# Kernel optimization log

Measured on AMD Instinct MI355X. Metric: run time of the kernel, lower is better.

## Reference

```python
import jax, jax.numpy as jnp
import numpy as np

DECAY = 0.1
ALPHA = 0.2
EPS = 1e-8


def setup_inputs() -> dict:
    key = jax.random.key(0)
    k1, k2, k3, k4 = jax.random.split(key, 4)
    B, S, N, V = 8, 1024, 64, 32000
    input_ids = jax.random.randint(k1, (B, S), 0, V)
    emb = jax.random.normal(k2, (V, N), dtype=jnp.float32)
    W = jax.random.normal(k3, (N, N, N), dtype=jnp.float32) * 0.05
    Wd = jax.random.normal(k4, (V, N), dtype=jnp.float32) * 0.02
    bd = jnp.zeros((V,), dtype=jnp.float32)
    return {"input_ids": input_ids, "emb": emb, "W": W, "Wd": Wd, "bd": bd}


def reference(input_ids, emb, W, Wd, bd):
    B, S = input_ids.shape
    N = W.shape[0]
    # Precompute relu(embedding) for all timesteps: [B, S, N]
    word = jax.nn.relu(emb[input_ids])

    def step(hidden, w_t):
        # hidden, w_t: [B, N]
        x = (1.0 - DECAY) * hidden + w_t
        interaction = jnp.einsum('ijk,bi,bj->bk', W, x, x)
        x_act = jax.nn.relu(x + ALPHA * interaction)
        h = x_act / (jnp.sum(x_act, axis=1, keepdims=True) + EPS)
        return h, h

    h0 = jnp.zeros((B, N), dtype=emb.dtype)
    hT, hs = jax.lax.scan(step, h0, jnp.swapaxes(word, 0, 1))  # hs: [S, B, N]
    # Decode every step: Linear(N -> V): h @ Wd.T + bd -> [B, S, V]
    logits = jnp.einsum('sbn,vn->bsv', hs, Wd) + bd
    return logits, hT
```

## Files before the change

kernel.cpp:

```cpp
#include <hip/hip_runtime.h>


typedef unsigned int u32;
typedef unsigned short u16;
typedef __attribute__((ext_vector_type(8))) short short8;
typedef __attribute__((ext_vector_type(4))) float f32x4;
typedef __attribute__((ext_vector_type(4))) int i32x4;

#define DECAY_ 0.1f
#define ALPHA_ 0.2f
#define EPS_ 1e-8f
#define B_ 8
#define S_ 1024
#define N_ 64
#define V_ 32000
#define NCHUNK_ 32
#define CHUNK_ 32
#define WARM_ 12
#define WBOUND_ 0.32f

static __device__ __forceinline__ u16 f2bf(float f) {
  u32 u = __float_as_uint(f);
  u32 r = (u + 0x7fffu + ((u >> 16) & 1u)) >> 16;
  return (u16)r;
}

#if defined(__has_builtin)
#if __has_builtin(__builtin_amdgcn_sdot4)
#define HAVE_SDOT4 1
#endif
#endif
static __device__ __forceinline__ int dot4(int a, int b, int c) {
#ifdef HAVE_SDOT4
  return __builtin_amdgcn_sdot4(a, b, c, false);
#else
  int s = c;
  s += (int)(signed char)(a) * (int)(signed char)(b);
  s += (int)(signed char)(a >> 8) * (int)(signed char)(b >> 8);
  s += (int)(signed char)(a >> 16) * (int)(signed char)(b >> 16);
  s += (int)(a >> 24) * (int)(b >> 24);
  return s;
#endif
}

static __device__ __forceinline__ float wave_max64(float v) {
#pragma unroll
  for (int m = 1; m < 64; m <<= 1) v = fmaxf(v, __shfl_xor(v, m, 64));
  return v;
}

__global__ void prep_kernel(const float* __restrict__ Wd, u16* __restrict__ wdb,
                            const float* __restrict__ W, u32* __restrict__ Wq) {
  int idx = blockIdx.x * blockDim.x + threadIdx.x;
  wdb[idx] = f2bf(Wd[idx]);
  if (blockIdx.x < 256) {
    const float s = 127.0f / WBOUND_;
    int j = idx >> 10;
    int q = (idx >> 6) & 15;
    int k = idx & 63;
    u32 pk = 0;
#pragma unroll
    for (int e = 0; e < 4; ++e) {
      float v = W[(((4 * q + e) * N_) + j) * N_ + k];
      int qi = (int)rintf(v * s);
      qi = qi > 127 ? 127 : (qi < -127 ? -127 : qi);
      pk |= ((u32)qi & 0xffu) << (8 * e);
    }
    int g = j >> 2, r = j & 3;
    int jX = g * 2 + (r & 1);
    int base = (r < 2) ? 0 : 32768;
    int q4 = q >> 2, e2 = q & 3;
    Wq[base + (((jX * 4 + q4) * 64 + k) << 2) + e2] = pk;
  }
}

__global__ __launch_bounds__(512, 2) void recur_kernel(
    const int* __restrict__ ids, const float* __restrict__ emb,
    const u32* __restrict__ Wq,
    u16* __restrict__ hs, float* __restrict__ outHT) {
  const int b = blockIdx.y;
  const int chunk = blockIdx.x;
  const int lane = threadIdx.x & 63;
  const int w = threadIdx.x >> 6;

  const int t0 = chunk * CHUNK_;
  const int ts = (chunk == 0) ? 0 : t0 - WARM_;
  const int tend = t0 + CHUNK_;

  __shared__ i32x4 lw[8192];
  __shared__ float part[8 * 64];
  __shared__ float xf_lds[N_];
  __shared__ u32 xq_lds[16];
  __shared__ float pend_w[2][N_];
  __shared__ float pend_b[2];

  const float sW = WBOUND_ * (1.0f / 127.0f);
  const i32x4* __restrict__ WqA = (const i32x4*)Wq;

  {
    const i32x4* src = (const i32x4*)(Wq + 32768);
    for (int ii = threadIdx.x; ii < 8192; ii += 512) lw[ii] = src[ii];
  }

  float xk = 0.0f, smul = 0.0f;

  if (w == 0) {
    int id0 = ids[b * S_ + ts];
    xk = fmaxf(emb[(size_t)id0 * N_ + lane], 0.0f);
    float bnd = fmaxf(wave_max64(xk), 1e-20f);
    smul = bnd * (1.0f / 127.0f) * sW;
    float inv = 127.0f / bnd;
    float u = xk * inv;
    float u0 = __shfl(u, (lane & 15) * 4 + 0, 64);
    float u1 = __shfl(u, (lane & 15) * 4 + 1, 64);
    float u2 = __shfl(u, (lane & 15) * 4 + 2, 64);
    float u3 = __shfl(u, (lane & 15) * 4 + 3, 64);
    xf_lds[lane] = xk;
    if (lane < 16) {
      xq_lds[lane] = (u32)(int)rintf(u0) | ((u32)(int)rintf(u1) << 8) |
                     ((u32)(int)rintf(u2) << 16) | ((u32)(int)rintf(u3) << 24);
    }
  }
  if (w == 1) {
    int i1 = ts + 1 < S_ ? ts + 1 : S_ - 1;
    int id1 = ids[b * S_ + i1];
    float pv = fmaxf(emb[(size_t)id1 * N_ + lane], 0.0f);
    float pm = wave_max64(pv);
    pend_w[(ts + 1) & 1][lane] = pv;
    if (lane == 0) pend_b[(ts + 1) & 1] = pm;
  }
  __syncthreads();

  for (int t = ts; t < tend; ++t) {
    float pv = 0.0f;
    if (w == 1) {
      int i2 = t + 2 < S_ ? t + 2 : S_ - 1;
      pv = emb[(size_t)ids[b * S_ + i2] * N_ + lane];
    }
    u32 pkv = xq_lds[lane & 15];
    int xr[16];
#pragma unroll
    for (int q = 0; q < 16; ++q) xr[q] = __builtin_amdgcn_readlane((int)pkv, q);
    float pf = 0.0f;
#pragma unroll
    for (int rr = 0; rr < 4; ++rr) {
      int a = 0;
#pragma unroll
      for (int q4 = 0; q4 < 4; ++q4) {
        i32x4 v = lw[((4 * w + rr) * 4 + q4) * 64 + lane];
        a = dot4(xr[4 * q4 + 0], v[0], a);
        a = dot4(xr[4 * q4 + 1], v[1], a);
        a = dot4(xr[4 * q4 + 2], v[2], a);
        a = dot4(xr[4 * q4 + 3], v[3], a);
      }
      int jb = (rr & 1) + ((rr & 2) << 1) + 2;
      pf += (float)a * xf_lds[8 * w + jb];
    }
#pragma unroll
    for (int rr = 0; rr < 4; ++rr) {
      int a = 0;
#pragma unroll
      for (int q4 = 0; q4 < 4; ++q4) {
        i32x4 v = WqA[((4 * w + rr) * 4 + q4) * 64 + lane];
        a = dot4(xr[4 * q4 + 0], v[0], a);
        a = dot4(xr[4 * q4 + 1], v[1], a);
        a = dot4(xr[4 * q4 + 2], v[2], a);
        a = dot4(xr[4 * q4 + 3], v[3], a);
      }
      int ja = (rr & 1) + ((rr & 2) << 1);
      pf += (float)a * xf_lds[8 * w + ja];
    }
    part[(w << 6) | lane] = pf;
    __syncthreads();

    if (w == 0) {
      float iact = 0.0f;
#pragma unroll
      for (int q = 0; q < 8; ++q) iact += part[(q << 6) | lane];
      float xact = fmaxf(fmaf(ALPHA_ * smul, iact, xk), 0.0f);
      float s = xact;
#pragma unroll
      for (int m = 1; m < 64; m <<= 1) s += __shfl_xor(s, m, 64);
      float rS = 1.0f / (s + EPS_);
      float h = xact * rS;

      if (t >= t0) {
        hs[((size_t)b * S_ + t) * N_ + lane] = f2bf(h);
        if (t == S_ - 1) outHT[b * N_ + lane] = h;
      }

      int rs = (t + 1) & 1;
      float wn = pend_w[rs][lane];
      float xn = fmaf(1.0f - DECAY_, h, wn);
      float nbnd = (1.0f - DECAY_) + pend_b[rs];
      float inv = 127.0f / nbnd;
      float u = xn * inv;
      float u0 = __shfl(u, (lane & 15) * 4 + 0, 64);
      float u1 = __shfl(u, (lane & 15) * 4 + 1, 64);
      float u2 = __shfl(u, (lane & 15) * 4 + 2, 64);
      float u3 = __shfl(u, (lane & 15) * 4 + 3, 64);
      xf_lds[lane] = xn;
      if (lane < 16) {
        xq_lds[lane] = (u32)(int)rintf(u0) | ((u32)(int)rintf(u1) << 8) |
                       ((u32)(int)rintf(u2) << 16) | ((u32)(int)rintf(u3) << 24);
      }
      smul = nbnd * (1.0f / 127.0f) * sW;
      xk = xn;
    } else if (w == 1) {
      float pr = fmaxf(pv, 0.0f);
      float pm = wave_max64(pr);
      pend_w[t & 1][lane] = pr;
      if (lane == 0) pend_b[t & 1] = pm;
    }
    __syncthreads();
  }
}

__global__ __launch_bounds__(512, 2) void decode_kernel(
    const u16* __restrict__ hs, const u16* __restrict__ wd,
    const float* __restrict__ bd, float* __restrict__ out) {
  const int lane = threadIdx.x & 63;
  const int w = threadIdx.x >> 6;
  const int wm = w >> 2, wn = w & 3;
  const int n0 = blockIdx.x * 128 + wn * 32;
  const int m0 = blockIdx.y * 128 + wm * 64;
  const int kg = (lane >> 4) * 8;
  const int rl = lane & 15;

  short8 bfr[2][2];
#pragma unroll
  for (int nt = 0; nt < 2; ++nt) {
    int v = n0 + nt * 16 + rl;
#pragma unroll
    for (int ks = 0; ks < 2; ++ks)
      bfr[nt][ks] = *(const short8*)(wd + (size_t)v * N_ + ks * 32 + kg);
  }
  short8 a[4][2];
#pragma unroll
  for (int mt = 0; mt < 4; ++mt) {
    int row = m0 + mt * 16 + rl;
#pragma unroll
    for (int ks = 0; ks < 2; ++ks)
      a[mt][ks] = *(const short8*)(hs + (size_t)row * N_ + ks * 32 + kg);
  }
  f32x4 acc[4][2];
#pragma unroll
  for (int nt = 0; nt < 2; ++nt) {
    float bdv = bd[n0 + nt * 16 + rl];
#pragma unroll
    for (int mt = 0; mt < 4; ++mt) acc[mt][nt] = {bdv, bdv, bdv, bdv};
  }
#pragma unroll
  for (int mt = 0; mt < 4; ++mt)
#pragma unroll
    for (int nt = 0; nt < 2; ++nt) {
      acc[mt][nt] =
          __builtin_amdgcn_mfma_f32_16x16x32_bf16(a[mt][0], bfr[nt][0], acc[mt][nt], 0, 0, 0);
      acc[mt][nt] =
          __builtin_amdgcn_mfma_f32_16x16x32_bf16(a[mt][1], bfr[nt][1], acc[mt][nt], 0, 0, 0);
    }
#pragma unroll
  for (int mt = 0; mt < 4; ++mt) {
    int rbase = m0 + mt * 16 + (lane >> 4) * 4;
#pragma unroll
    for (int i = 0; i < 4; ++i) {
      float* op = out + (size_t)(rbase + i) * V_ + n0 + rl;
      __builtin_nontemporal_store(acc[mt][0][i], op);
      __builtin_nontemporal_store(acc[mt][1][i], op + 16);
    }
  }
}

extern "C" void kernel_launch(void* const* d_in, const int* in_sizes, int n_in,
                              void* d_out, int out_size, void* d_ws, size_t ws_size,
                              hipStream_t stream) {
  const int* ids = (const int*)d_in[0];
  const float* emb = (const float*)d_in[1];
  const float* W = (const float*)d_in[2];
  const float* Wd = (const float*)d_in[3];
  const float* bd = (const float*)d_in[4];
  float* out = (float*)d_out;
  char* ws = (char*)d_ws;

  u32* Wq = (u32*)(ws);
  u16* hs = (u16*)(ws + 262144);
  u16* wdb = (u16*)(ws + 1310720);

  hipLaunchKernelGGL(prep_kernel, dim3(8000), dim3(256), 0, stream, Wd, wdb, W, Wq);
  hipLaunchKernelGGL(recur_kernel, dim3(NCHUNK_, B_), dim3(512), 0, stream, ids, emb,
                     Wq, hs, out + (size_t)B_ * S_ * V_);
  hipLaunchKernelGGL(decode_kernel, dim3(V_ / 128, (B_ * S_) / 128), dim3(512), 0, stream,
                     hs, wdb, bd, out);

  (void)in_sizes; (void)n_in; (void)out_size; (void)ws_size;
}
```

Measured before the change: 294.4 us.

## Symmetrize bilinear weight tensor to halve recurrence dot-product work

The cubic interaction x^T W_k x is rewritten with a symmetrized upper-triangular tensor U (U_ij = W_ij + W_ji for i<j, W_ii on the diagonal), so each step does about half the int8 dot products. The packed triangle (about 147 KB) fits wholly in LDS, which removes the per-step global/L2 reads of half of W. Because symmetrized entries have a larger range, the quantization bound is raised, which costs int8 precision. The triangular loop also spreads work unevenly across lanes of different m.

```diff
diff --git a/kernel.cpp b/kernel.cpp
--- a/kernel.cpp
+++ b/kernel.cpp
@@ -17,7 +17,9 @@
 #define NCHUNK_ 32
 #define CHUNK_ 32
 #define WARM_ 12
-#define WBOUND_ 0.32f
+#define UBOUND_ 0.45f
+#define NUNITS_ 288
+#define UQ_DWORDS_ (NUNITS_ * 64 * 2)
 
 static __device__ __forceinline__ u16 f2bf(float f) {
   u32 u = __float_as_uint(f);
@@ -50,33 +52,40 @@
 }
 
 __global__ void prep_kernel(const float* __restrict__ Wd, u16* __restrict__ wdb,
-                            const float* __restrict__ W, u32* __restrict__ Wq) {
+                            const float* __restrict__ W, u32* __restrict__ Uq) {
   int idx = blockIdx.x * blockDim.x + threadIdx.x;
   wdb[idx] = f2bf(Wd[idx]);
-  if (blockIdx.x < 256) {
-    const float s = 127.0f / WBOUND_;
-    int j = idx >> 10;
-    int q = (idx >> 6) & 15;
-    int k = idx & 63;
-    u32 pk = 0;
-#pragma unroll
-    for (int e = 0; e < 4; ++e) {
-      float v = W[(((4 * q + e) * N_) + j) * N_ + k];
-      int qi = (int)rintf(v * s);
-      qi = qi > 127 ? 127 : (qi < -127 ? -127 : qi);
-      pk |= ((u32)qi & 0xffu) << (8 * e);
-    }
-    int g = j >> 2, r = j & 3;
-    int jX = g * 2 + (r & 1);
-    int base = (r < 2) ? 0 : 32768;
-    int q4 = q >> 2, e2 = q & 3;
-    Wq[base + (((jX * 4 + q4) * 64 + k) << 2) + e2] = pk;
+  if (blockIdx.x < 64) {
+    const int j = blockIdx.x;
+    const int m = j >> 3;
+    const int off8 = j + 4 * m * (m - 1) + (j & 7) * m;
+    const int cnt = 2 * (m + 1) * 64;
+    const float s = 127.0f / UBOUND_;
+    for (int d = threadIdx.x; d < cnt; d += 256) {
+      int q4 = d >> 6;
+      int k = d & 63;
+      u32 pk = 0;
+#pragma unroll
+      for (int e = 0; e < 4; ++e) {
+        int i = 4 * q4 + e;
+        float v = 0.0f;
+        if (i < j)
+          v = W[((size_t)i * N_ + j) * N_ + k] + W[((size_t)j * N_ + i) * N_ + k];
+        else if (i == j)
+          v = W[((size_t)j * N_ + j) * N_ + k];
+        int qi = (int)rintf(v * s);
+        qi = qi > 127 ? 127 : (qi < -127 ? -127 : qi);
+        pk |= ((u32)qi & 0xffu) << (8 * e);
+      }
+      int dst = 2 * ((off8 + (q4 >> 1)) * 64 + k) + (q4 & 1);
+      Uq[dst] = pk;
+    }
   }
 }
 
 __global__ __launch_bounds__(512, 2) void recur_kernel(
     const int* __restrict__ ids, const float* __restrict__ emb,
-    const u32* __restrict__ Wq,
+    const u32* __restrict__ Uq,
     u16* __restrict__ hs, float* __restrict__ outHT) {
   const int b = blockIdx.y;
   const int chunk = blockIdx.x;
@@ -87,19 +96,19 @@
   const int ts = (chunk == 0) ? 0 : t0 - WARM_;
   const int tend = t0 + CHUNK_;
 
-  __shared__ i32x4 lw[8192];
+  __shared__ int2 lw2[NUNITS_ * 64];
   __shared__ float part[8 * 64];
   __shared__ float xf_lds[N_];
   __shared__ u32 xq_lds[16];
   __shared__ float pend_w[2][N_];
   __shared__ float pend_b[2];
 
-  const float sW = WBOUND_ * (1.0f / 127.0f);
-  const i32x4* __restrict__ WqA = (const i32x4*)Wq;
+  const float sW = UBOUND_ * (1.0f / 127.0f);
 
   {
-    const i32x4* src = (const i32x4*)(Wq + 32768);
-    for (int ii = threadIdx.x; ii < 8192; ii += 512) lw[ii] = src[ii];
+    const i32x4* src = (const i32x4*)Uq;
+    i32x4* dst = (i32x4*)lw2;
+    for (int ii = threadIdx.x; ii < UQ_DWORDS_ / 4; ii += 512) dst[ii] = src[ii];
   }
 
   float xk = 0.0f, smul = 0.0f;
@@ -143,32 +152,17 @@
     for (int q = 0; q < 16; ++q) xr[q] = __builtin_amdgcn_readlane((int)pkv, q);
     float pf = 0.0f;
 #pragma unroll
-    for (int rr = 0; rr < 4; ++rr) {
+    for (int m = 0; m < 8; ++m) {
+      const int j = w + 8 * m;
+      const int off8 = j + 4 * m * (m - 1) + w * m;
       int a = 0;
 #pragma unroll
-      for (int q4 = 0; q4 < 4; ++q4) {
-        i32x4 v = lw[((4 * w + rr) * 4 + q4) * 64 + lane];
-        a = dot4(xr[4 * q4 + 0], v[0], a);
-        a = dot4(xr[4 * q4 + 1], v[1], a);
-        a = dot4(xr[4 * q4 + 2], v[2], a);
-        a = dot4(xr[4 * q4 + 3], v[3], a);
-      }
-      int jb = (rr & 1) + ((rr & 2) << 1) + 2;
-      pf += (float)a * xf_lds[8 * w + jb];
-    }
-#pragma unroll
-    for (int rr = 0; rr < 4; ++rr) {
-      int a = 0;
-#pragma unroll
-      for (int q4 = 0; q4 < 4; ++q4) {
-        i32x4 v = WqA[((4 * w + rr) * 4 + q4) * 64 + lane];
-        a = dot4(xr[4 * q4 + 0], v[0], a);
-        a = dot4(xr[4 * q4 + 1], v[1], a);
-        a = dot4(xr[4 * q4 + 2], v[2], a);
-        a = dot4(xr[4 * q4 + 3], v[3], a);
-      }
-      int ja = (rr & 1) + ((rr & 2) << 1);
-      pf += (float)a * xf_lds[8 * w + ja];
+      for (int u = 0; u <= m; ++u) {
+        int2 v = lw2[(off8 + u) * 64 + lane];
+        a = dot4(xr[2 * u], v.x, a);
+        a = dot4(xr[2 * u + 1], v.y, a);
+      }
+      pf += (float)a * xf_lds[j];
     }
     part[(w << 6) | lane] = pf;
     __syncthreads();
@@ -282,13 +276,13 @@
   float* out = (float*)d_out;
   char* ws = (char*)d_ws;
 
-  u32* Wq = (u32*)(ws);
-  u16* hs = (u16*)(ws + 262144);
-  u16* wdb = (u16*)(ws + 1310720);
-
-  hipLaunchKernelGGL(prep_kernel, dim3(8000), dim3(256), 0, stream, Wd, wdb, W, Wq);
+  u32* Uq = (u32*)(ws);
+  u16* hs = (u16*)(ws + 147456);
+  u16* wdb = (u16*)(ws + 1196032);
+
+  hipLaunchKernelGGL(prep_kernel, dim3(8000), dim3(256), 0, stream, Wd, wdb, W, Uq);
   hipLaunchKernelGGL(recur_kernel, dim3(NCHUNK_, B_), dim3(512), 0, stream, ids, emb,
-                     Wq, hs, out + (size_t)B_ * S_ * V_);
+                     Uq, hs, out + (size_t)B_ * S_ * V_);
   hipLaunchKernelGGL(decode_kernel, dim3(V_ / 128, (B_ * S_) / 128), dim3(512), 0, stream,
                      hs, wdb, bd, out);
 
```

Result: no change. 296.7 us (+0.8%).
